# Performance work log

Hardware: AMD Instinct MI355X
Metric: run time of the kernel (lower is better)

## Reference

```python
import jax, jax.numpy as jnp
import numpy as np

# Dims: N batch, I input channels, C = in/hidden/attention/projection/out channels (all 128),
# streams=1, groups=1, spatial kernel 3, dropout 0.
N, I, C, H, W = 8, 128, 128, 36, 36


def _conv(x, w, pad):
    # x: [N, Cin, H, W], w: [Cout, Cin, kh, kw]
    return jax.lax.conv_general_dilated(
        x, w, (1, 1), pad, dimension_numbers=("NCHW", "OIHW", "NCHW"))


def _bias(b):
    return b[None, :, None, None]


def setup_inputs() -> dict:
    key = jax.random.key(0)
    ks = jax.random.split(key, 16)
    std = 0.05

    def w(k, o, i, s):
        return jax.random.normal(k, (o, i, s, s), jnp.float32) * std

    p = {}
    p["inp"] = jax.random.normal(ks[0], (N, I, H, W), jnp.float32)
    p["c0"] = jax.random.normal(ks[1], (1, C, 1, 1), jnp.float32)
    # proj_x: 1x1 conv input->in_channels, bias init 0
    p["w_x"] = w(ks[2], C, I, 1)
    p["b_x"] = jnp.zeros((C,), jnp.float32)
    # token convs (3x3, no bias); q uses SAME pad, k/v VALID
    p["w_qx"] = w(ks[3], C, C, 3)
    p["w_qc"] = w(ks[4], C, C, 3)
    scale = C ** (-0.5)  # gain = attn_channels^-0.5 on k projections
    p["w_kx"] = w(ks[5], C, C, 3) * scale
    p["w_kc"] = w(ks[6], C, C, 3) * scale
    p["w_vx"] = w(ks[7], C, C, 3)
    p["w_vc"] = w(ks[8], C, C, 3)
    # gating 1x1 convs: proj_z (bias=init_gate=1), proj_n (bias=0), in 2*proj channels
    p["w_z"] = w(ks[9], C, 2 * C, 1)
    p["b_z"] = jnp.ones((C,), jnp.float32)
    p["w_n"] = w(ks[10], C, 2 * C, 1)
    p["b_n"] = jnp.zeros((C,), jnp.float32)
    # proj_h: in_channels + 2*projection_channels -> hidden
    p["w_h"] = w(ks[11], C, 3 * C, 1)
    p["b_h"] = jnp.zeros((C,), jnp.float32)
    # output 1x1 conv hidden -> out_channels
    p["w_o"] = w(ks[12], C, C, 1)
    p["b_o"] = jnp.zeros((C,), jnp.float32)
    return p


def reference(inp, c0, w_x, b_x, w_qx, w_qc, w_kx, w_kc, w_vx, w_vc,
              w_z, b_z, w_n, b_n, w_h, b_h, w_o, b_o):
    # proj_x (1x1) -> x: [N, C, H, W]
    x = _conv(inp, w_x, "VALID") + _bias(b_x)
    n_, _, hh, ww = x.shape
    c = jnp.broadcast_to(c0, (n_, c0.shape[1], hh, ww))
    q_len = hh * ww
    # q: SAME pad -> Q = H*W tokens; k/v: VALID -> D = (H-2)*(W-2) tokens
    q = jnp.stack([_conv(x, w_qx, "SAME"), _conv(c, w_qc, "SAME")], 0)
    q = q.reshape(2, n_, -1, q_len)                      # [A, N, C, Q]
    k_x = _conv(x, w_kx, "VALID")
    d_len = k_x.shape[2] * k_x.shape[3]
    k = jnp.stack([k_x, _conv(c, w_kc, "VALID")], 0).reshape(2, n_, -1, d_len)   # [B, N, C, D]
    v = jnp.stack([_conv(x, w_vx, "VALID"), _conv(c, w_vc, "VALID")], 0)
    v = v.reshape(2, n_, -1, d_len)                      # [B, N, C, D]
    # all (A query source) x (B key/value source) attention pairs
    attn = jax.nn.softmax(jnp.einsum("ancq,bncd->anbqd", q, k), axis=-1)
    a = jnp.einsum("bncd,anbqd->anbcq", v, attn)         # [A, N, B, C, Q]
    a = a.reshape(2, n_, -1, hh, ww)                     # channels = B*C = 2*proj
    a_x, a_c = a[0], a[1]
    # GRU-style gated cell update (stored state; not part of the returned output)
    z = jax.nn.sigmoid(_conv(a_c, w_z, "VALID") + _bias(b_z))
    n_cand = jnp.tanh(_conv(a_c, w_n, "VALID") + _bias(b_n))
    c_new = z * c + (1.0 - z) * n_cand  # noqa: F841 (past['c'] in the original)
    # hidden: tanh(proj_h(cat[x, a_x])), dropout p=0 is identity
    xa = jnp.concatenate([x, a_x], axis=1)               # [N, 3*C, H, W]
    h = jnp.tanh(_conv(xa, w_h, "VALID") + _bias(b_h))
    return _conv(h, w_o, "VALID") + _bias(b_o)           # [N, C, H, W]
```

## Files before the change

kernel.cpp:

```cpp
#include <hip/hip_runtime.h>
#include <hip/hip_bf16.h>
#include <math.h>

#define NN 8
#define CH 128
#define HH 36
#define WWI 36
#define PP 1296
#define DD 1156
#define VP 1280
#define KC 1152
#define QT 81
#define DT 5
#define XPP 1444

typedef __attribute__((ext_vector_type(8))) short short8;
typedef __attribute__((ext_vector_type(4))) float f32x4;
typedef __attribute__((ext_vector_type(8))) _Float16 half8;

__device__ inline unsigned short f2bf(float f) {
    __hip_bfloat16 h = __float2bfloat16(f);
    return __builtin_bit_cast(unsigned short, h);
}
__device__ inline float fast_tanh(float x) {
    float e = __expf(2.f * x);
    return 1.f - 2.f / (e + 1.f);
}
#define MFMA(a, b, c) __builtin_amdgcn_mfma_f32_16x16x32_bf16((a), (b), (c), 0, 0, 0)
#define GLDS(g, l) __builtin_amdgcn_global_load_lds( \
    (const __attribute__((address_space(1))) unsigned int*)(g), \
    (__attribute__((address_space(3))) unsigned int*)(l), 16, 0, 0)

__global__ __launch_bounds__(256)
void k_setup(const float* __restrict__ wq, const float* __restrict__ wk,
             const float* __restrict__ wv, const float* __restrict__ wh,
             const float* __restrict__ wo, const float* __restrict__ wx,
             const float* __restrict__ c0, const float* __restrict__ w_vc,
             const float* __restrict__ b_h,
             unsigned short* __restrict__ wcat, unsigned short* __restrict__ whb,
             unsigned short* __restrict__ wob,
             float* __restrict__ hconst,
             const float* __restrict__ inp, const float* __restrict__ bx,
             unsigned short* __restrict__ xp)
{
    const int b = blockIdx.x;
    if (b >= 565) {
        const int n = b - 565;
        unsigned short* xpn = xp + (size_t)n * XPP * CH;
        for (int e = threadIdx.x; e < 148 * 16; e += 256) {
            int cell = e >> 4, part = e & 15;
            int y, x;
            if (cell < 38)       { y = 0;              x = cell; }
            else if (cell < 76)  { y = 37;             x = cell - 38; }
            else if (cell < 112) { y = cell - 76 + 1;  x = 0; }
            else                 { y = cell - 112 + 1; x = 37; }
            *(uint4*)&xpn[((size_t)(y * 38 + x)) * CH + part * 8] = make_uint4(0, 0, 0, 0);
        }
        return;
    }
    if (b >= 241) {
        const int t = threadIdx.x;
        const int wave = t >> 6, lane = t & 63;
        const int pid = (b - 241) * 4 + wave;
        const int n = pid / 162;
        const int rem = pid - n * 162;
        const int by = rem / 81;
        const int qg = rem - by * 81;
        const int quad = lane >> 4, lrow = lane & 15;
        const int p0 = qg * 16;
        const int co0 = by * 64;
        const float* in_n = inp + (size_t)n * CH * PP;
        f32x4 acc[4] = {};

#pragma unroll
        for (int ks = 0; ks < 4; ++ks) {
            union { short8 v; unsigned short u[8]; } a;
            int ci0 = ks * 32 + quad * 8;
#pragma unroll
            for (int j = 0; j < 8; ++j)
                a.u[j] = f2bf(in_n[(size_t)(ci0 + j) * PP + p0 + lrow]);
#pragma unroll
            for (int ni = 0; ni < 4; ++ni) {
                const float* wrow = wx + (size_t)(co0 + ni * 16 + lrow) * CH + ks * 32 + quad * 8;
                float4 f0 = *(const float4*)wrow;
                float4 f1 = *(const float4*)(wrow + 4);
                union { short8 v; unsigned short u[8]; } bb;
                bb.u[0] = f2bf(f0.x); bb.u[1] = f2bf(f0.y);
                bb.u[2] = f2bf(f0.z); bb.u[3] = f2bf(f0.w);
                bb.u[4] = f2bf(f1.x); bb.u[5] = f2bf(f1.y);
                bb.u[6] = f2bf(f1.z); bb.u[7] = f2bf(f1.w);
                acc[ni] = MFMA(a.v, bb.v, acc[ni]);
            }
        }
        unsigned short* xn = xp + (size_t)n * XPP * CH;
#pragma unroll
        for (int ni = 0; ni < 4; ++ni) {
            float bv = bx[co0 + ni * 16 + lrow];
#pragma unroll
            for (int r = 0; r < 4; ++r) {
                int p = p0 + quad * 4 + r;
                int off = ((p / 36 + 1) * 38 + (p % 36) + 1) * CH;
                xn[(size_t)off + co0 + ni * 16 + lrow] = f2bf(acc[ni][r] + bv);
            }
        }
        return;
    }
    if (b == 240) {
        __shared__ float c0s[CH];
        __shared__ float part[256];
        __shared__ float vcs[CH];
        const int t = threadIdx.x;
        const int c = t & 127, half = t >> 7;
        if (t < CH) c0s[t] = c0[t];
        __syncthreads();
        {
            const float* row = w_vc + (size_t)c * 1152 + half * 576;
            float s = 0.f;
#pragma unroll 4
            for (int j4 = 0; j4 < 144; ++j4) {
                float4 v = ((const float4*)row)[j4];
                int j = half * 576 + j4 * 4;
                s += v.x * c0s[j / 9] + v.y * c0s[(j + 1) / 9]
                   + v.z * c0s[(j + 2) / 9] + v.w * c0s[(j + 3) / 9];
            }
            part[t] = s;
        }
        __syncthreads();
        if (t < CH) vcs[t] = part[t] + part[t + 128];
        __syncthreads();
        {
            const float* wrow = wh + (size_t)c * 384 + 256 + half * 64;
            float hs = 0.f;
#pragma unroll
            for (int j4 = 0; j4 < 16; ++j4) {
                float4 v = ((const float4*)wrow)[j4];
                int ci = half * 64 + j4 * 4;
                hs += v.x * vcs[ci] + v.y * vcs[ci + 1] + v.z * vcs[ci + 2] + v.w * vcs[ci + 3];
            }
            part[t] = hs;
        }
        __syncthreads();
        if (t < CH) hconst[t] = b_h[t] + part[t] + part[t + 128];
        return;
    }
    const int tid = threadIdx.x;
    if (b >= 224) {
        int i0 = ((b - 224) * 256 + tid) * 4;
        float4 v = *(const float4*)&wo[i0];
        wob[i0 + 0] = f2bf(v.x); wob[i0 + 1] = f2bf(v.y);
        wob[i0 + 2] = f2bf(v.z); wob[i0 + 3] = f2bf(v.w);
        return;
    }
    if (b >= 192) {
        int i0 = ((b - 192) * 256 + tid) * 4;
        int c2 = i0 >> 8, k2 = i0 & 255;
        float4 v = *(const float4*)&wh[(size_t)c2 * 384 + k2];
        whb[i0 + 0] = f2bf(v.x); whb[i0 + 1] = f2bf(v.y);
        whb[i0 + 2] = f2bf(v.z); whb[i0 + 3] = f2bf(v.w);
        return;
    }
    int t = b * 256 + tid;
    int tensor = t >> 14;
    int rem = t & 16383;
    int co = rem >> 7, ci = rem & 127;
    const float* srcw = (tensor == 0 ? wq : tensor == 1 ? wk : wv)
                        + (size_t)co * KC + ci * 9;
    unsigned short* dst = wcat + (size_t)tensor * 147456 + (size_t)co * KC + ci;
    float f[9];
#pragma unroll
    for (int k = 0; k < 9; ++k) f[k] = srcw[k];
#pragma unroll
    for (int k = 0; k < 9; ++k) dst[k * 128] = f2bf(f[k]);
}

__global__ __launch_bounds__(256)
void k_conv(const unsigned short* __restrict__ xp, const unsigned short* __restrict__ wcat,
            unsigned short* __restrict__ qt, unsigned short* __restrict__ kt,
            unsigned short* __restrict__ vb)
{
    __shared__ unsigned short lA[3][2048];
    __shared__ unsigned short lB[3][4096];
    const int t = threadIdx.x;
    const int wave = t >> 6, lane = t & 63;
    const int quad = lane >> 4, lrow = lane & 15;
    const int mode = blockIdx.y;
    const int n = blockIdx.z;
    const int limit = (mode == 0) ? PP : DD;
    const int tile0 = blockIdx.x * 64;
    if (tile0 >= limit) return;
    const unsigned short* xn = xp + (size_t)n * XPP * CH;
    const unsigned short* wb = wcat + (size_t)mode * 128 * KC;

    const int aseg = t & 3;
    int apr, apc;
    {
        int tok = tile0 + (t >> 2); if (tok >= limit) tok = limit - 1;
        int dv = (mode == 0) ? 36 : 34;
        apr = tok / dv; apc = tok - apr * dv;
        if (mode != 0) { apr += 1; apc += 1; }
    }
    const unsigned short* wbr0 = wb + (size_t)(wave * 16 + (lane >> 2)) * KC + (lane & 3) * 8;
    const unsigned short* wbr1 = wb + (size_t)(64 + wave * 16 + (lane >> 2)) * KC + (lane & 3) * 8;
    const int ldsA = wave * 512;
    const int ldsB0 = wave * 512;
    const int ldsB1 = 2048 + wave * 512;

    auto stage = [&](int ks, int buf) {
        int tap = ks >> 2;
        int ky = tap / 3, kx = tap - ky * 3;
        int ci = (ks & 3) * 32 + aseg * 8;
        const unsigned short* srcA = xn + ((size_t)((apr + ky) * 38 + apc + kx)) * CH + ci;
        int koff = tap * 128 + (ks & 3) * 32;
        GLDS(srcA, &lA[buf][ldsA]);
        GLDS(wbr0 + koff, &lB[buf][ldsB0]);
        GLDS(wbr1 + koff, &lB[buf][ldsB1]);
    };

    f32x4 acc[4][2] = {};
    stage(0, 0);
    stage(1, 1);
    stage(2, 2);

#pragma unroll
    for (int ks = 0; ks < 36; ++ks) {
        if (ks < 34)      asm volatile("s_waitcnt vmcnt(6)" ::: "memory");
        else if (ks == 34) asm volatile("s_waitcnt vmcnt(3)" ::: "memory");
        else               asm volatile("s_waitcnt vmcnt(0)" ::: "memory");
        __builtin_amdgcn_sched_barrier(0);
        __builtin_amdgcn_s_barrier();
        __builtin_amdgcn_sched_barrier(0);
        const int buf = ks % 3;
        short8 b0 = *(const short8*)&lB[buf][(wave * 32 + lrow) * 32 + quad * 8];
        short8 b1 = *(const short8*)&lB[buf][(wave * 32 + 16 + lrow) * 32 + quad * 8];
#pragma unroll
        for (int mi = 0; mi < 4; ++mi) {
            short8 a = *(const short8*)&lA[buf][(mi * 16 + lrow) * 32 + quad * 8];
            acc[mi][0] = MFMA(a, b0, acc[mi][0]);
            acc[mi][1] = MFMA(a, b1, acc[mi][1]);
        }
        __builtin_amdgcn_sched_barrier(0);
        __builtin_amdgcn_s_barrier();
        __builtin_amdgcn_sched_barrier(0);
        if (ks < 33) stage(ks + 3, buf);
    }

    if (mode == 0) {
        unsigned short* qn = qt + (size_t)n * PP * CH;
#pragma unroll
        for (int mi = 0; mi < 4; ++mi)
#pragma unroll
            for (int r = 0; r < 4; ++r) {
                int p = tile0 + mi * 16 + quad * 4 + r;
                if (p < PP)
#pragma unroll
                    for (int ni = 0; ni < 2; ++ni)
                        qn[(size_t)p * CH + (wave * 2 + ni) * 16 + lrow] = f2bf(acc[mi][ni][r]);
            }
    } else if (mode == 1) {
        unsigned short* kn = kt + (size_t)n * DD * CH;
#pragma unroll
        for (int mi = 0; mi < 4; ++mi)
#pragma unroll
            for (int r = 0; r < 4; ++r) {
                int d = tile0 + mi * 16 + quad * 4 + r;
                if (d < DD)
#pragma unroll
                    for (int ni = 0; ni < 2; ++ni)
                        kn[(size_t)d * CH + (wave * 2 + ni) * 16 + lrow] = f2bf(acc[mi][ni][r]);
            }
    } else {
        unsigned short* vn = vb + (size_t)n * CH * VP;
#pragma unroll
        for (int mi = 0; mi < 4; ++mi)
#pragma unroll
            for (int r = 0; r < 4; ++r) {
                int d = tile0 + mi * 16 + quad * 4 + r;
                if (d < DD)
#pragma unroll
                    for (int ni = 0; ni < 2; ++ni)
                        vn[(size_t)((wave * 2 + ni) * 16 + lrow) * VP + d] = f2bf(acc[mi][ni][r]);
            }
    }
}

__global__ __launch_bounds__(256)
void k_attn(const unsigned short* __restrict__ qt, const unsigned short* __restrict__ kt,
            const unsigned short* __restrict__ vb, _Float16* __restrict__ po,
            float* __restrict__ pm, float* __restrict__ pl)
{
    __shared__ unsigned short lS[2][128 * 40];
    __shared__ unsigned short lp[4][16 * 136];
    const int t = threadIdx.x;
    const int wave = t >> 6, lane = t & 63;
    const int quad = lane >> 4, lrow = lane & 15;
    const int qg = blockIdx.x;
    const int dt = blockIdx.y;
    const int n = blockIdx.z;
    const int qti = qg * 4 + wave;
    const int d0 = dt * 256;
    const unsigned short* qn = qt + (size_t)n * PP * CH;
    const unsigned short* kn = kt + (size_t)n * DD * CH;
    const unsigned short* vn = vb + (size_t)n * CH * VP;

    const int arow = t >> 2, aseg8 = (t & 3) * 8;
    const int lo0 = arow * 40 + aseg8;
    const int lo1 = (arow + 64) * 40 + aseg8;

    short8 qa[4];
    {
        int qrow = qti * 16 + lrow; if (qrow >= PP) qrow = PP - 1;
#pragma unroll
        for (int ks = 0; ks < 4; ++ks)
            qa[ks] = *(const short8*)&qn[(size_t)qrow * CH + ks * 32 + quad * 8];
    }

    f32x4 o[8] = {};
    float mx[4] = {-1e30f, -1e30f, -1e30f, -1e30f};
    float rs[4] = {0.f, 0.f, 0.f, 0.f};

#pragma unroll
    for (int h = 0; h < 2; ++h) {
        const int dbase = d0 + h * 128;
        int kr0 = dbase + arow;      if (kr0 >= DD) kr0 = DD - 1;
        int kr1 = dbase + arow + 64; if (kr1 >= DD) kr1 = DD - 1;
        const unsigned short* kp0 = kn + (size_t)kr0 * CH + aseg8;
        const unsigned short* kp1 = kn + (size_t)kr1 * CH + aseg8;
        const unsigned short* vp0 = vn + (size_t)arow * VP + dbase + aseg8;
        const unsigned short* vp1 = vn + (size_t)(arow + 64) * VP + dbase + aseg8;

        f32x4 s[8] = {};
        uint4 r0 = *(const uint4*)kp0;
        uint4 r1 = *(const uint4*)kp1;
        *(uint4*)&lS[0][lo0] = r0;
        *(uint4*)&lS[0][lo1] = r1;
        __syncthreads();
#pragma unroll
        for (int ks = 0; ks < 4; ++ks) {
            const int buf = ks & 1;
            if (ks < 3) {
                r0 = *(const uint4*)(kp0 + (ks + 1) * 32);
                r1 = *(const uint4*)(kp1 + (ks + 1) * 32);
            }
#pragma unroll
            for (int ni = 0; ni < 8; ++ni) {
                short8 b = *(const short8*)&lS[buf][(ni * 16 + lrow) * 40 + quad * 8];
                s[ni] = MFMA(qa[ks], b, s[ni]);
            }
            if (ks < 3) {
                *(uint4*)&lS[buf ^ 1][lo0] = r0;
                *(uint4*)&lS[buf ^ 1][lo1] = r1;
            }
            __syncthreads();
        }

#pragma unroll
        for (int ni = 0; ni < 8; ++ni)
            if (dbase + ni * 16 + lrow >= DD)
#pragma unroll
                for (int r = 0; r < 4; ++r) s[ni][r] = -1e30f;

        float hm[4] = {-1e30f, -1e30f, -1e30f, -1e30f};
#pragma unroll
        for (int ni = 0; ni < 8; ++ni)
#pragma unroll
            for (int r = 0; r < 4; ++r) hm[r] = fmaxf(hm[r], s[ni][r]);
#pragma unroll
        for (int off = 1; off < 16; off <<= 1)
#pragma unroll
            for (int r = 0; r < 4; ++r) hm[r] = fmaxf(hm[r], __shfl_xor(hm[r], off, 64));

        float m[4], sc[4];
#pragma unroll
        for (int r = 0; r < 4; ++r) {
            m[r] = fmaxf(mx[r], hm[r]);
            sc[r] = __expf(mx[r] - m[r]);
        }

        float hs[4] = {0.f, 0.f, 0.f, 0.f};
#pragma unroll
        for (int ni = 0; ni < 8; ++ni)
#pragma unroll
            for (int r = 0; r < 4; ++r) {
                float e = __expf(s[ni][r] - m[r]);
                s[ni][r] = e;
                hs[r] += e;
            }
#pragma unroll
        for (int off = 1; off < 16; off <<= 1)
#pragma unroll
            for (int r = 0; r < 4; ++r) hs[r] += __shfl_xor(hs[r], off, 64);
#pragma unroll
        for (int r = 0; r < 4; ++r) {
            rs[r] = rs[r] * sc[r] + hs[r];
            mx[r] = m[r];
        }
#pragma unroll
        for (int ni = 0; ni < 8; ++ni)
#pragma unroll
            for (int r = 0; r < 4; ++r) o[ni][r] *= sc[r];

#pragma unroll
        for (int ni = 0; ni < 8; ++ni)
#pragma unroll
            for (int r = 0; r < 4; ++r)
                lp[wave][(quad * 4 + r) * 136 + ni * 16 + lrow] = f2bf(s[ni][r]);

        r0 = *(const uint4*)vp0;
        r1 = *(const uint4*)vp1;
        *(uint4*)&lS[0][lo0] = r0;
        *(uint4*)&lS[0][lo1] = r1;
        __syncthreads();
#pragma unroll
        for (int ks = 0; ks < 4; ++ks) {
            const int buf = ks & 1;
            if (ks < 3) {
                r0 = *(const uint4*)(vp0 + (ks + 1) * 32);
                r1 = *(const uint4*)(vp1 + (ks + 1) * 32);
            }
            short8 pa = *(const short8*)&lp[wave][lrow * 136 + ks * 32 + quad * 8];
#pragma unroll
            for (int ni = 0; ni < 8; ++ni) {
                short8 b = *(const short8*)&lS[buf][(ni * 16 + lrow) * 40 + quad * 8];
                o[ni] = MFMA(pa, b, o[ni]);
            }
            if (ks < 3) {
                *(uint4*)&lS[buf ^ 1][lo0] = r0;
                *(uint4*)&lS[buf ^ 1][lo1] = r1;
            }
            __syncthreads();
        }
    }

    if (qti < QT) {
        const int base = (n * QT + qti) * DT + dt;
        _Float16* pob = po + (size_t)base * 2048;
#pragma unroll
        for (int ni = 0; ni < 8; ++ni)
#pragma unroll
            for (int r = 0; r < 4; ++r)
                pob[(quad * 4 + r) * 128 + ni * 16 + lrow] = (_Float16)o[ni][r];
        if (lrow == 0)
#pragma unroll
            for (int r = 0; r < 4; ++r) {
                pm[base * 16 + quad * 4 + r] = mx[r];
                pl[base * 16 + quad * 4 + r] = rs[r];
            }
    }
}

__global__ __launch_bounds__(256)
void k_ahout(const _Float16* __restrict__ po, const float* __restrict__ pm,
             const float* __restrict__ pl, const unsigned short* __restrict__ xp,
             const unsigned short* __restrict__ whb, const float* __restrict__ hconst,
             const unsigned short* __restrict__ wob, const float* __restrict__ bo,
             float* __restrict__ out)
{
    __shared__ float sm[80], ssc[80], smg[16], sli[16];
    __shared__ unsigned short la0[16 * 136];
    __shared__ unsigned short lh[16 * 136];
    const int qti = blockIdx.x;
    const int n = blockIdx.y;
    const int base = (n * QT + qti) * DT;
    const int t = threadIdx.x;

    if (t < 80) sm[t] = pm[base * 16 + t];
    __syncthreads();
    if (t < 16) {
        float mg = -1e30f;
#pragma unroll
        for (int dt = 0; dt < DT; ++dt) mg = fmaxf(mg, sm[dt * 16 + t]);
        float ls = 0.f;
#pragma unroll
        for (int dt = 0; dt < DT; ++dt) ls += __expf(sm[dt * 16 + t] - mg) * pl[base * 16 + dt * 16 + t];
        smg[t] = mg; sli[t] = 1.f / ls;
    }
    __syncthreads();
    if (t < 80) ssc[t] = __expf(sm[t] - smg[t & 15]);
    __syncthreads();
    {
        const int row = t >> 4;
        const int c0 = (t & 15) * 8;
        float acc[8] = {};
#pragma unroll
        for (int dt = 0; dt < DT; ++dt) {
            half8 v = *(const half8*)&po[(size_t)(base + dt) * 2048 + t * 8];
            float scv = ssc[dt * 16 + row];
#pragma unroll
            for (int j = 0; j < 8; ++j) acc[j] += scv * (float)v[j];
        }
        float inv = sli[row];
#pragma unroll
        for (int j = 0; j < 8; ++j)
            la0[row * 136 + c0 + j] = f2bf(acc[j] * inv);
    }
    __syncthreads();

    const int wave = t >> 6, lane = t & 63;
    const int quad = lane >> 4, lrow = lane & 15;
    const int p0 = qti * 16;
    const unsigned short* x0 = xp + (size_t)n * XPP * CH;
    const int ptok = p0 + lrow;
    const int xoff = ((ptok / 36 + 1) * 38 + (ptok % 36) + 1) * CH;

    f32x4 acc1[2] = {};
#pragma unroll
    for (int ks = 0; ks < 8; ++ks) {
        int col = (ks & 3) * 32 + quad * 8;
        short8 a;
        if (ks < 4) a = *(const short8*)&x0[(size_t)xoff + col];
        else        a = *(const short8*)&la0[lrow * 136 + col];
#pragma unroll
        for (int j = 0; j < 2; ++j) {
            int ni = wave * 2 + j;
            short8 b = *(const short8*)&whb[(size_t)(ni * 16 + lrow) * 256 + ks * 32 + quad * 8];
            acc1[j] = MFMA(a, b, acc1[j]);
        }
    }
#pragma unroll
    for (int j = 0; j < 2; ++j) {
        int ni = wave * 2 + j;
        float hc = hconst[ni * 16 + lrow];
#pragma unroll
        for (int r = 0; r < 4; ++r)
            lh[(quad * 4 + r) * 136 + ni * 16 + lrow] = f2bf(fast_tanh(acc1[j][r] + hc));
    }
    __syncthreads();

    f32x4 acc2[2] = {};
#pragma unroll
    for (int ks = 0; ks < 4; ++ks) {
        short8 a = *(const short8*)&lh[lrow * 136 + ks * 32 + quad * 8];
#pragma unroll
        for (int j = 0; j < 2; ++j) {
            int ni = wave * 2 + j;
            short8 b = *(const short8*)&wob[(size_t)(ni * 16 + lrow) * CH + ks * 32 + quad * 8];
            acc2[j] = MFMA(a, b, acc2[j]);
        }
    }
#pragma unroll
    for (int j = 0; j < 2; ++j) {
        int ni = wave * 2 + j;
        float bv = bo[ni * 16 + lrow];
#pragma unroll
        for (int r = 0; r < 4; ++r)
            out[((size_t)(n * CH + ni * 16 + lrow)) * PP + p0 + quad * 4 + r] = acc2[j][r] + bv;
    }
}

extern "C" void kernel_launch(void* const* d_in, const int* in_sizes, int n_in,
                              void* d_out, int out_size, void* d_ws, size_t ws_size,
                              hipStream_t stream)
{
    const float* inp  = (const float*)d_in[0];
    const float* c0   = (const float*)d_in[1];
    const float* w_x  = (const float*)d_in[2];
    const float* b_x  = (const float*)d_in[3];
    const float* w_qx = (const float*)d_in[4];
    const float* w_kx = (const float*)d_in[6];
    const float* w_vx = (const float*)d_in[8];
    const float* w_vc = (const float*)d_in[9];
    const float* w_h  = (const float*)d_in[14];
    const float* b_h  = (const float*)d_in[15];
    const float* w_o  = (const float*)d_in[16];
    const float* b_o  = (const float*)d_in[17];
    float* out = (float*)d_out;

    char* w = (char*)d_ws;
    unsigned short* xp   = (unsigned short*)(w);
    unsigned short* qt   = (unsigned short*)(w + 2957312);
    unsigned short* kt   = (unsigned short*)(w + 5611520);
    unsigned short* vb   = (unsigned short*)(w + 7979008);
    unsigned short* wcat = (unsigned short*)(w + 10600448);
    unsigned short* whb  = (unsigned short*)(w + 11485184);
    unsigned short* wob  = (unsigned short*)(w + 11550720);
    float* hconst        = (float*)(w + 11583488);
    float* pm            = (float*)(w + 11616256);
    float* pl            = (float*)(w + 11824128);
    _Float16* po         = (_Float16*)(w + 12031488);

    hipLaunchKernelGGL(k_setup, dim3(573), dim3(256), 0, stream,
                       w_qx, w_kx, w_vx, w_h, w_o, w_x, c0, w_vc, b_h,
                       wcat, whb, wob, hconst, inp, b_x, xp);

    hipLaunchKernelGGL(k_conv, dim3(21, 3, NN), dim3(256), 0, stream, xp, wcat, qt, kt, vb);

    hipLaunchKernelGGL(k_attn, dim3(21, DT, NN), dim3(256), 0, stream, qt, kt, vb, po, pm, pl);

    hipLaunchKernelGGL(k_ahout, dim3(QT, NN), dim3(256), 0, stream,
                       po, pm, pl, xp, whb, hconst, wob, b_o, out);
}
```

Measured before the change: 182.8 us.

## Fuse K and V 3x3 convs into one block sharing the input tile

```diff
diff --git a/kernel.cpp b/kernel.cpp
--- a/kernel.cpp
+++ b/kernel.cpp
@@ -178,8 +178,7 @@
             unsigned short* __restrict__ qt, unsigned short* __restrict__ kt,
             unsigned short* __restrict__ vb)
 {
-    __shared__ unsigned short lA[3][2048];
-    __shared__ unsigned short lB[3][4096];
+    __shared__ unsigned short pool[20480];
     const int t = threadIdx.x;
     const int wave = t >> 6, lane = t & 63;
     const int quad = lane >> 4, lrow = lane & 15;
@@ -189,7 +188,6 @@
     const int tile0 = blockIdx.x * 64;
     if (tile0 >= limit) return;
     const unsigned short* xn = xp + (size_t)n * XPP * CH;
-    const unsigned short* wb = wcat + (size_t)mode * 128 * KC;
 
     const int aseg = t & 3;
     int apr, apc;
@@ -199,52 +197,55 @@
         apr = tok / dv; apc = tok - apr * dv;
         if (mode != 0) { apr += 1; apc += 1; }
     }
-    const unsigned short* wbr0 = wb + (size_t)(wave * 16 + (lane >> 2)) * KC + (lane & 3) * 8;
-    const unsigned short* wbr1 = wb + (size_t)(64 + wave * 16 + (lane >> 2)) * KC + (lane & 3) * 8;
-    const int ldsA = wave * 512;
-    const int ldsB0 = wave * 512;
-    const int ldsB1 = 2048 + wave * 512;
-
-    auto stage = [&](int ks, int buf) {
-        int tap = ks >> 2;
-        int ky = tap / 3, kx = tap - ky * 3;
-        int ci = (ks & 3) * 32 + aseg * 8;
-        const unsigned short* srcA = xn + ((size_t)((apr + ky) * 38 + apc + kx)) * CH + ci;
-        int koff = tap * 128 + (ks & 3) * 32;
-        GLDS(srcA, &lA[buf][ldsA]);
-        GLDS(wbr0 + koff, &lB[buf][ldsB0]);
-        GLDS(wbr1 + koff, &lB[buf][ldsB1]);
-    };
-
-    f32x4 acc[4][2] = {};
-    stage(0, 0);
-    stage(1, 1);
-    stage(2, 2);
-
-#pragma unroll
-    for (int ks = 0; ks < 36; ++ks) {
-        if (ks < 34)      asm volatile("s_waitcnt vmcnt(6)" ::: "memory");
-        else if (ks == 34) asm volatile("s_waitcnt vmcnt(3)" ::: "memory");
-        else               asm volatile("s_waitcnt vmcnt(0)" ::: "memory");
-        __builtin_amdgcn_sched_barrier(0);
-        __builtin_amdgcn_s_barrier();
-        __builtin_amdgcn_sched_barrier(0);
-        const int buf = ks % 3;
-        short8 b0 = *(const short8*)&lB[buf][(wave * 32 + lrow) * 32 + quad * 8];
-        short8 b1 = *(const short8*)&lB[buf][(wave * 32 + 16 + lrow) * 32 + quad * 8];
-#pragma unroll
-        for (int mi = 0; mi < 4; ++mi) {
-            short8 a = *(const short8*)&lA[buf][(mi * 16 + lrow) * 32 + quad * 8];
-            acc[mi][0] = MFMA(a, b0, acc[mi][0]);
-            acc[mi][1] = MFMA(a, b1, acc[mi][1]);
-        }
-        __builtin_amdgcn_sched_barrier(0);
-        __builtin_amdgcn_s_barrier();
-        __builtin_amdgcn_sched_barrier(0);
-        if (ks < 33) stage(ks + 3, buf);
-    }
+    const int rowsel = (lane >> 2);
+    const int segoff = (lane & 3) * 8;
 
     if (mode == 0) {
+        const unsigned short* wb = wcat;
+        const unsigned short* wbr0 = wb + (size_t)(wave * 16 + rowsel) * KC + segoff;
+        const unsigned short* wbr1 = wb + (size_t)(64 + wave * 16 + rowsel) * KC + segoff;
+
+        auto stage = [&](int ks, int buf) {
+            int tap = ks >> 2;
+            int ky = tap / 3, kx = tap - ky * 3;
+            int ci = (ks & 3) * 32 + aseg * 8;
+            const unsigned short* srcA = xn + ((size_t)((apr + ky) * 38 + apc + kx)) * CH + ci;
+            int koff = tap * 128 + (ks & 3) * 32;
+            GLDS(srcA, pool + buf * 2048 + wave * 512);
+            GLDS(wbr0 + koff, pool + 6144 + buf * 4096 + wave * 512);
+            GLDS(wbr1 + koff, pool + 6144 + buf * 4096 + 2048 + wave * 512);
+        };
+
+        f32x4 acc[4][2] = {};
+        stage(0, 0);
+        stage(1, 1);
+        stage(2, 2);
+
+#pragma unroll
+        for (int ks = 0; ks < 36; ++ks) {
+            if (ks < 34)      asm volatile("s_waitcnt vmcnt(6)" ::: "memory");
+            else if (ks == 34) asm volatile("s_waitcnt vmcnt(3)" ::: "memory");
+            else               asm volatile("s_waitcnt vmcnt(0)" ::: "memory");
+            __builtin_amdgcn_sched_barrier(0);
+            __builtin_amdgcn_s_barrier();
+            __builtin_amdgcn_sched_barrier(0);
+            const int buf = ks % 3;
+            const unsigned short* lB = pool + 6144 + buf * 4096;
+            const unsigned short* lA = pool + buf * 2048;
+            short8 b0 = *(const short8*)&lB[(wave * 32 + lrow) * 32 + quad * 8];
+            short8 b1 = *(const short8*)&lB[(wave * 32 + 16 + lrow) * 32 + quad * 8];
+#pragma unroll
+            for (int mi = 0; mi < 4; ++mi) {
+                short8 a = *(const short8*)&lA[(mi * 16 + lrow) * 32 + quad * 8];
+                acc[mi][0] = MFMA(a, b0, acc[mi][0]);
+                acc[mi][1] = MFMA(a, b1, acc[mi][1]);
+            }
+            __builtin_amdgcn_sched_barrier(0);
+            __builtin_amdgcn_s_barrier();
+            __builtin_amdgcn_sched_barrier(0);
+            if (ks < 33) stage(ks + 3, buf);
+        }
+
         unsigned short* qn = qt + (size_t)n * PP * CH;
 #pragma unroll
         for (int mi = 0; mi < 4; ++mi)
@@ -256,29 +257,75 @@
                     for (int ni = 0; ni < 2; ++ni)
                         qn[(size_t)p * CH + (wave * 2 + ni) * 16 + lrow] = f2bf(acc[mi][ni][r]);
             }
-    } else if (mode == 1) {
+    } else {
+        const unsigned short* wbk = wcat + (size_t)1 * 128 * KC;
+        const unsigned short* wbv = wcat + (size_t)2 * 128 * KC;
+        const unsigned short* wbrk0 = wbk + (size_t)(wave * 16 + rowsel) * KC + segoff;
+        const unsigned short* wbrk1 = wbk + (size_t)(64 + wave * 16 + rowsel) * KC + segoff;
+        const unsigned short* wbrv0 = wbv + (size_t)(wave * 16 + rowsel) * KC + segoff;
+        const unsigned short* wbrv1 = wbv + (size_t)(64 + wave * 16 + rowsel) * KC + segoff;
+
+        auto stage = [&](int ks, int buf) {
+            int tap = ks >> 2;
+            int ky = tap / 3, kx = tap - ky * 3;
+            int ci = (ks & 3) * 32 + aseg * 8;
+            const unsigned short* srcA = xn + ((size_t)((apr + ky) * 38 + apc + kx)) * CH + ci;
+            int koff = tap * 128 + (ks & 3) * 32;
+            GLDS(srcA, pool + buf * 2048 + wave * 512);
+            GLDS(wbrk0 + koff, pool + 4096 + buf * 4096 + wave * 512);
+            GLDS(wbrk1 + koff, pool + 4096 + buf * 4096 + 2048 + wave * 512);
+            GLDS(wbrv0 + koff, pool + 12288 + buf * 4096 + wave * 512);
+            GLDS(wbrv1 + koff, pool + 12288 + buf * 4096 + 2048 + wave * 512);
+        };
+
+        f32x4 acck[4][2] = {};
+        f32x4 accv[4][2] = {};
+        stage(0, 0);
+        stage(1, 1);
+
+#pragma unroll
+        for (int ks = 0; ks < 36; ++ks) {
+            if (ks < 35) asm volatile("s_waitcnt vmcnt(5)" ::: "memory");
+            else         asm volatile("s_waitcnt vmcnt(0)" ::: "memory");
+            __builtin_amdgcn_sched_barrier(0);
+            __builtin_amdgcn_s_barrier();
+            __builtin_amdgcn_sched_barrier(0);
+            const int buf = ks & 1;
+            const unsigned short* lA = pool + buf * 2048;
+            const unsigned short* lBk = pool + 4096 + buf * 4096;
+            const unsigned short* lBv = pool + 12288 + buf * 4096;
+            short8 bk0 = *(const short8*)&lBk[(wave * 32 + lrow) * 32 + quad * 8];
+            short8 bk1 = *(const short8*)&lBk[(wave * 32 + 16 + lrow) * 32 + quad * 8];
+            short8 bv0 = *(const short8*)&lBv[(wave * 32 + lrow) * 32 + quad * 8];
+            short8 bv1 = *(const short8*)&lBv[(wave * 32 + 16 + lrow) * 32 + quad * 8];
+#pragma unroll
+            for (int mi = 0; mi < 4; ++mi) {
+                short8 a = *(const short8*)&lA[(mi * 16 + lrow) * 32 + quad * 8];
+                acck[mi][0] = MFMA(a, bk0, acck[mi][0]);
+                acck[mi][1] = MFMA(a, bk1, acck[mi][1]);
+                accv[mi][0] = MFMA(a, bv0, accv[mi][0]);
+                accv[mi][1] = MFMA(a, bv1, accv[mi][1]);
+            }
+            __builtin_amdgcn_sched_barrier(0);
+            __builtin_amdgcn_s_barrier();
+            __builtin_amdgcn_sched_barrier(0);
+            if (ks < 34) stage(ks + 2, buf);
+        }
+
         unsigned short* kn = kt + (size_t)n * DD * CH;
+        unsigned short* vn = vb + (size_t)n * CH * VP;
 #pragma unroll
         for (int mi = 0; mi < 4; ++mi)
 #pragma unroll
             for (int r = 0; r < 4; ++r) {
                 int d = tile0 + mi * 16 + quad * 4 + r;
-                if (d < DD)
-#pragma unroll
-                    for (int ni = 0; ni < 2; ++ni)
-                        kn[(size_t)d * CH + (wave * 2 + ni) * 16 + lrow] = f2bf(acc[mi][ni][r]);
-            }
-    } else {
-        unsigned short* vn = vb + (size_t)n * CH * VP;
-#pragma unroll
-        for (int mi = 0; mi < 4; ++mi)
-#pragma unroll
-            for (int r = 0; r < 4; ++r) {
-                int d = tile0 + mi * 16 + quad * 4 + r;
-                if (d < DD)
-#pragma unroll
-                    for (int ni = 0; ni < 2; ++ni)
-                        vn[(size_t)((wave * 2 + ni) * 16 + lrow) * VP + d] = f2bf(acc[mi][ni][r]);
+                if (d < DD) {
+#pragma unroll
+                    for (int ni = 0; ni < 2; ++ni) {
+                        kn[(size_t)d * CH + (wave * 2 + ni) * 16 + lrow] = f2bf(acck[mi][ni][r]);
+                        vn[(size_t)((wave * 2 + ni) * 16 + lrow) * VP + d] = f2bf(accv[mi][ni][r]);
+                    }
+                }
             }
     }
 }
@@ -582,7 +629,7 @@
                        w_qx, w_kx, w_vx, w_h, w_o, w_x, c0, w_vc, b_h,
                        wcat, whb, wob, hconst, inp, b_x, xp);
 
-    hipLaunchKernelGGL(k_conv, dim3(21, 3, NN), dim3(256), 0, stream, xp, wcat, qt, kt, vb);
+    hipLaunchKernelGGL(k_conv, dim3(21, 2, NN), dim3(256), 0, stream, xp, wcat, qt, kt, vb);
 
     hipLaunchKernelGGL(k_attn, dim3(21, DT, NN), dim3(256), 0, stream, qt, kt, vb, po, pm, pl);
 
```

Result: no change. 186.1 us (+1.8%).
